# Kernel tuning notes

Hardware: AMD Instinct MI355X
Metric: run time of the kernel (lower is better)

## Reference

```python
import jax, jax.numpy as jnp
import numpy as np

T, H, F, E, K = 4096, 2048, 1408, 8, 2  # tokens, hidden, intermediate, experts, top_k


def setup_inputs() -> dict:
    key = jax.random.key(0)
    k1, k2, k3, k4 = jax.random.split(key, 4)
    return {
        "hidden_states": jax.random.normal(k1, (T, H), dtype=jnp.float32),
        "router_logits": jax.random.normal(k2, (T, E), dtype=jnp.float32),
        # w1: (E, 2, H, F) where dim 1 = [gate_proj, up_proj]
        "w1": jax.random.normal(k3, (E, 2, H, F), dtype=jnp.float32) * 0.02,
        # w2: (E, F, H) down projection
        "w2": jax.random.normal(k4, (E, F, H), dtype=jnp.float32) * 0.02,
        "top_k": K,
    }


def reference(hidden_states, router_logits, w1, w2, top_k):
    # Router: softmax over all experts, then select top_k.
    # renormalize_topk_logits=False -> combine weights are the raw softmax probs.
    probs = jax.nn.softmax(router_logits, axis=-1)            # (T, E)
    topk_w, topk_ids = jax.lax.top_k(probs, top_k)            # (T, K) each

    num_experts = w1.shape[0]
    out = jnp.zeros_like(hidden_states)                       # (T, H)
    # Fixed small loop over experts (structurally distinct weight slices);
    # each expert's FFN is a dense GEMM over all tokens, masked by the
    # per-token combine coefficient (0 for tokens not routed to this expert).
    for e in range(num_experts):
        coef = jnp.sum(jnp.where(topk_ids == e, topk_w, 0.0), axis=-1)  # (T,)
        gate = hidden_states @ w1[e, 0]                       # (T, F)
        up = hidden_states @ w1[e, 1]                         # (T, F)
        h = jax.nn.silu(gate) * up                            # SwiGLU
        out = out + coef[:, None] * (h @ w2[e])               # (T, H)
    return out
```

## Files before the change

### kernel.cpp

```cpp
#include <hip/hip_runtime.h>
#include <stdint.h>

#define T_TOK 4096
#define HID   2048
#define FF    1408
#define NE    8
#define BUF   16384
#define NT1   (HID / 32)
#define NT2   (FF / 32)

typedef __attribute__((ext_vector_type(8))) short short8;
typedef __attribute__((ext_vector_type(4))) float f32x4;

__device__ inline unsigned short f2bf(float f) {
  uint32_t u = __builtin_bit_cast(uint32_t, f);
  u += 0x7fffu + ((u >> 16) & 1u);
  return (unsigned short)(u >> 16);
}

__device__ inline uint32_t cvt_pk(float a, float b) {
  uint32_t r;
  asm("v_cvt_pk_bf16_f32 %0, %1, %2" : "=v"(r) : "v"(a), "v"(b));
  return r;
}

__device__ inline void gload16(const void* g, void* l) {
  __builtin_amdgcn_global_load_lds(
      (const __attribute__((address_space(1))) unsigned int*)g,
      (__attribute__((address_space(3))) unsigned int*)l, 16, 0, 0);
}

__device__ inline void wait8_barrier() {
  asm volatile("s_waitcnt vmcnt(8)" ::: "memory");
  __builtin_amdgcn_s_barrier();
  asm volatile("" ::: "memory");
}
__device__ inline void wait4_barrier() {
  asm volatile("s_waitcnt vmcnt(4)" ::: "memory");
  __builtin_amdgcn_s_barrier();
  asm volatile("" ::: "memory");
}
__device__ inline void wait0_barrier() {
  asm volatile("s_waitcnt vmcnt(0)" ::: "memory");
  __builtin_amdgcn_s_barrier();
  asm volatile("" ::: "memory");
}

__global__ __launch_bounds__(256) void route_kernel(const float* __restrict__ logits,
                                                    int2* __restrict__ eids,
                                                    float2* __restrict__ ecfs) {
  int t = blockIdx.x * 256 + threadIdx.x;
  const float4* lp = (const float4*)(logits + (size_t)t * NE);
  float4 a = lp[0], b = lp[1];
  float l[8] = {a.x, a.y, a.z, a.w, b.x, b.y, b.z, b.w};
  float mx = l[0];
#pragma unroll
  for (int i = 1; i < 8; ++i) mx = fmaxf(mx, l[i]);
  float s = 0.f, p[8];
#pragma unroll
  for (int i = 0; i < 8; ++i) { p[i] = __expf(l[i] - mx); s += p[i]; }
  float inv = 1.f / s;
  int e0 = 0;
#pragma unroll
  for (int i = 1; i < 8; ++i) if (l[i] > l[e0]) e0 = i;
  int e1 = (e0 == 0) ? 1 : 0;
#pragma unroll
  for (int i = 0; i < 8; ++i) if (i != e0 && l[i] > l[e1]) e1 = i;
  eids[t] = make_int2(e0, e1);
  ecfs[t] = make_float2(p[e0] * inv, p[e1] * inv);
}

__global__ __launch_bounds__(256) void compact_kernel(const int2* __restrict__ eids,
                                                      const float2* __restrict__ ecfs,
                                                      int* __restrict__ tok,
                                                      float* __restrict__ coef,
                                                      int* __restrict__ rowptr,
                                                      int* __restrict__ invm) {
  int e = blockIdx.x, tid = threadIdx.x;
  __shared__ int hist[8];
  __shared__ int wsum[4];
  __shared__ int runv;
  if (tid < 8) hist[tid] = 0;
  __syncthreads();
  for (int t = tid; t < T_TOK; t += 256) {
    int2 ei = eids[t];
    atomicAdd(&hist[ei.x], 1);
    atomicAdd(&hist[ei.y], 1);
  }
  __syncthreads();
  int off = 0;
  for (int j = 0; j < e; ++j) off += hist[j];
  if (tid == 0) {
    runv = 0;
    if (e == 0) rowptr[0] = 0;
    rowptr[e + 1] = off + hist[e];
  }
  __syncthreads();
  int wave = tid >> 6, lane = tid & 63;
  for (int c = 0; c < T_TOK; c += 256) {
    int t = c + tid;
    int2 ei = eids[t];
    float2 cf = ecfs[t];
    bool fl = false; float cv = 0.f; int ks = 0;
    if (ei.x == e)      { fl = true; cv = cf.x; ks = 0; }
    else if (ei.y == e) { fl = true; cv = cf.y; ks = 1; }
    unsigned long long m = __ballot(fl);
    if (lane == 0) wsum[wave] = __popcll(m);
    __syncthreads();
    int woff = runv;
    for (int wv = 0; wv < wave; ++wv) woff += wsum[wv];
    int pos = off + woff + __popcll(m & ((1ull << lane) - 1ull));
    if (fl) { tok[pos] = t; coef[pos] = cv; invm[2 * t + ks] = pos; }
    __syncthreads();
    if (tid == 0) runv += wsum[0] + wsum[1] + wsum[2] + wsum[3];
    __syncthreads();
  }
}

__global__ __launch_bounds__(256) void cvtx_kernel(const float* __restrict__ x,
                                                   unsigned short* __restrict__ xb) {
  int i = blockIdx.x * 256 + threadIdx.x;
  float4 v = ((const float4*)x)[i];
  uint2 o;
  o.x = cvt_pk(v.x, v.y);
  o.y = cvt_pk(v.z, v.w);
  ((uint2*)xb)[i] = o;
}

__global__ __launch_bounds__(256) void wcvt_kernel(const float* __restrict__ in,
                                                   unsigned short* __restrict__ out,
                                                   int R, int C) {
  __shared__ unsigned short t[64][72];
  const float* ip = in + ((size_t)blockIdx.z * R + blockIdx.y * 64) * C + blockIdx.x * 64;
  int tid = threadIdx.x;
  int r = tid >> 2, cg = (tid & 3) * 16;
  const float* rp = ip + (size_t)r * C + cg;
#pragma unroll
  for (int j = 0; j < 4; ++j) {
    float4 v = *(const float4*)(rp + j * 4);
    int c = cg + j * 4;
    t[c + 0][r] = f2bf(v.x);
    t[c + 1][r] = f2bf(v.y);
    t[c + 2][r] = f2bf(v.z);
    t[c + 3][r] = f2bf(v.w);
  }
  __syncthreads();
  int cr = tid >> 2, kg = (tid & 3) * 16;
  unsigned short* op = out + ((size_t)blockIdx.z * C + blockIdx.x * 64 + cr) * R +
                       blockIdx.y * 64 + kg;
  *(short8*)op = *(const short8*)&t[cr][kg];
  *(short8*)(op + 8) = *(const short8*)&t[cr][kg + 8];
}

__global__ __launch_bounds__(256) void gemm1_kernel(const unsigned short* __restrict__ Xb,
                                                    const unsigned short* __restrict__ w1t,
                                                    const int* __restrict__ tok,
                                                    const int* __restrict__ rowptr,
                                                    unsigned short* __restrict__ hbuf) {
  int f = blockIdx.x + 22 * blockIdx.y;
  int g = (f & 7) * 88 + (f >> 3);
  int ftile = g >> 5, mtile = g & 31;
  int e = blockIdx.z;
  int base = rowptr[e], cnt = rowptr[e + 1] - base;
  if (mtile * 128 >= cnt) return;
  __shared__ char smem[4 * BUF];
  int tid = threadIdx.x, lane = tid & 63, wave = tid >> 6;

  int rA = wave * 32 + (lane >> 2);
  int cd = (lane & 3) ^ ((rA >> 1) & 3);
  int sA0 = min(mtile * 128 + rA, cnt - 1);
  int sA1 = min(mtile * 128 + rA + 16, cnt - 1);
  const unsigned short* gA0 = Xb + (size_t)tok[base + sA0] * HID + cd * 8;
  const unsigned short* gA1 = Xb + (size_t)tok[base + sA1] * HID + cd * 8;
  int r1 = rA + 16;
  int p0 = (rA >> 4) & 1, f0 = (rA & 15) + 16 * (rA >> 5);
  int p1 = (r1 >> 4) & 1, f1 = (r1 & 15) + 16 * (r1 >> 5);
  const unsigned short* gB0 = w1t + ((size_t)(e * 2 + p0) * FF + ftile * 64 + f0) * HID + cd * 8;
  const unsigned short* gB1 = w1t + ((size_t)(e * 2 + p1) * FF + ftile * 64 + f1) * HID + cd * 8;
  int lb = wave * 2048 + lane * 16;

#define STG1(bp, k0) do {                          \
    gload16(gA0 + (k0), (bp) + lb);                \
    gload16(gA1 + (k0), (bp) + lb + 1024);         \
    gload16(gB0 + (k0), (bp) + 8192 + lb);         \
    gload16(gB1 + (k0), (bp) + 8192 + lb + 1024);  \
  } while (0)

  int wm = wave >> 1, wn = wave & 1, kc = lane >> 4;
  int aoff[4], boff[4];
#pragma unroll
  for (int mi = 0; mi < 4; ++mi) {
    int row = wm * 64 + mi * 16 + (lane & 15);
    aoff[mi] = row * 64 + ((kc ^ ((row >> 1) & 3)) << 4);
  }
#pragma unroll
  for (int ni = 0; ni < 4; ++ni) {
    int n = wn * 64 + ni * 16 + (lane & 15);
    boff[ni] = 8192 + n * 64 + ((kc ^ ((n >> 1) & 3)) << 4);
  }

  const f32x4 vz = {0.f, 0.f, 0.f, 0.f};
  f32x4 acc[4][4];
#pragma unroll
  for (int mi = 0; mi < 4; ++mi)
#pragma unroll
    for (int ni = 0; ni < 4; ++ni) acc[mi][ni] = vz;

  STG1(smem, 0);
  STG1(smem + BUF, 32);
  STG1(smem + 2 * BUF, 64);
  wait8_barrier();

  for (int t = 0; t < NT1; ++t) {
    char* cur = smem + (t & 3) * BUF;
    bool pf = (t + 3) < NT1;
    if (pf) STG1(smem + ((t + 3) & 3) * BUF, (t + 3) * 32);
    short8 af[4], bb[4];
#pragma unroll
    for (int mi = 0; mi < 4; ++mi) af[mi] = *(const short8*)(cur + aoff[mi]);
#pragma unroll
    for (int ni = 0; ni < 4; ++ni) bb[ni] = *(const short8*)(cur + boff[ni]);
    __builtin_amdgcn_s_setprio(1);
#pragma unroll
    for (int mi = 0; mi < 4; ++mi)
#pragma unroll
      for (int ni = 0; ni < 4; ++ni)
        acc[mi][ni] = __builtin_amdgcn_mfma_f32_16x16x32_bf16(af[mi], bb[ni], acc[mi][ni], 0, 0, 0);
    __builtin_amdgcn_s_setprio(0);
    if (pf) wait8_barrier();
    else if (t + 2 < NT1) wait4_barrier();
    else wait0_barrier();
  }
#undef STG1

  int fb = ftile * 64 + wn * 32 + (lane & 15);
#pragma unroll
  for (int mi = 0; mi < 4; ++mi) {
#pragma unroll
    for (int i = 0; i < 4; ++i) {
      int ml = wm * 64 + mi * 16 + (lane >> 4) * 4 + i;
      int slot = mtile * 128 + ml;
      if (slot < cnt) {
        size_t hrow = (size_t)(base + slot) * FF + fb;
        float g0 = acc[mi][0][i], u0 = acc[mi][1][i];
        float g1 = acc[mi][2][i], u1 = acc[mi][3][i];
        hbuf[hrow]      = f2bf(g0 / (1.f + __expf(-g0)) * u0);
        hbuf[hrow + 16] = f2bf(g1 / (1.f + __expf(-g1)) * u1);
      }
    }
  }
}

__global__ __launch_bounds__(256) void gemm2_kernel(const unsigned short* __restrict__ hbuf,
                                                    const unsigned short* __restrict__ w2t,
                                                    const int* __restrict__ rowptr,
                                                    float* __restrict__ obuf) {
  int f = blockIdx.x + 16 * blockIdx.y;
  int g = (f & 7) * 64 + (f >> 3);
  int ntile = g >> 5, mtile = g & 31;
  int e = blockIdx.z;
  int base = rowptr[e], cnt = rowptr[e + 1] - base;
  if (mtile * 128 >= cnt) return;
  __shared__ char smem[3 * BUF];
  int tid = threadIdx.x, lane = tid & 63, wave = tid >> 6;

  int rA = wave * 32 + (lane >> 2);
  int cd = (lane & 3) ^ ((rA >> 1) & 3);
  int sA0 = min(mtile * 128 + rA, cnt - 1);
  int sA1 = min(mtile * 128 + rA + 16, cnt - 1);
  const unsigned short* gA0 = hbuf + (size_t)(base + sA0) * FF + cd * 8;
  const unsigned short* gA1 = hbuf + (size_t)(base + sA1) * FF + cd * 8;
  const unsigned short* gB0 = w2t + ((size_t)e * HID + ntile * 128 + rA) * FF + cd * 8;
  const unsigned short* gB1 = gB0 + (size_t)16 * FF;
  int lb = wave * 2048 + lane * 16;

#define STG2(bp, k0) do {                          \
    gload16(gA0 + (k0), (bp) + lb);                \
    gload16(gA1 + (k0), (bp) + lb + 1024);         \
    gload16(gB0 + (k0), (bp) + 8192 + lb);         \
    gload16(gB1 + (k0), (bp) + 8192 + lb + 1024);  \
  } while (0)

  int wm = wave >> 1, wn = wave & 1, kc = lane >> 4;
  int aoff[4], boff[4];
#pragma unroll
  for (int mi = 0; mi < 4; ++mi) {
    int row = wm * 64 + mi * 16 + (lane & 15);
    aoff[mi] = row * 64 + ((kc ^ ((row >> 1) & 3)) << 4);
  }
#pragma unroll
  for (int ni = 0; ni < 4; ++ni) {
    int n = wn * 64 + ni * 16 + (lane & 15);
    boff[ni] = 8192 + n * 64 + ((kc ^ ((n >> 1) & 3)) << 4);
  }

  const f32x4 vz = {0.f, 0.f, 0.f, 0.f};
  f32x4 acc[4][4];
#pragma unroll
  for (int mi = 0; mi < 4; ++mi)
#pragma unroll
    for (int ni = 0; ni < 4; ++ni) acc[mi][ni] = vz;

  STG2(smem, 0);
  STG2(smem + BUF, 32);
  wait4_barrier();

  char* cur = smem;
  char* nxt = smem + 2 * BUF;
  for (int t = 0; t < NT2; ++t) {
    bool pf = (t + 2) < NT2;
    if (pf) STG2(nxt, (t + 2) * 32);
    short8 af[4], bb[4];
#pragma unroll
    for (int mi = 0; mi < 4; ++mi) af[mi] = *(const short8*)(cur + aoff[mi]);
#pragma unroll
    for (int ni = 0; ni < 4; ++ni) bb[ni] = *(const short8*)(cur + boff[ni]);
    __builtin_amdgcn_s_setprio(1);
#pragma unroll
    for (int mi = 0; mi < 4; ++mi)
#pragma unroll
      for (int ni = 0; ni < 4; ++ni)
        acc[mi][ni] = __builtin_amdgcn_mfma_f32_16x16x32_bf16(af[mi], bb[ni], acc[mi][ni], 0, 0, 0);
    __builtin_amdgcn_s_setprio(0);
    if (pf) wait4_barrier(); else wait0_barrier();
    cur = (cur == smem + 2 * BUF) ? smem : cur + BUF;
    nxt = (nxt == smem + 2 * BUF) ? smem : nxt + BUF;
  }
#undef STG2

  int nb = ntile * 128 + wn * 64 + (lane & 15);
#pragma unroll
  for (int mi = 0; mi < 4; ++mi) {
#pragma unroll
    for (int i = 0; i < 4; ++i) {
      int ml = wm * 64 + mi * 16 + (lane >> 4) * 4 + i;
      int slot = mtile * 128 + ml;
      if (slot < cnt) {
        float* op = obuf + (size_t)(base + slot) * HID + nb;
#pragma unroll
        for (int ni = 0; ni < 4; ++ni) op[ni * 16] = acc[mi][ni][i];
      }
    }
  }
}

__global__ __launch_bounds__(256) void combine_kernel(const float* __restrict__ obuf,
                                                      const int2* __restrict__ invm,
                                                      const float* __restrict__ coef,
                                                      float* __restrict__ out) {
  int idx = blockIdx.x * 256 + threadIdx.x;
  int t = idx >> 9, h4 = idx & 511;
  int2 pp = invm[t];
  float c0 = coef[pp.x], c1 = coef[pp.y];
  float4 a = ((const float4*)(obuf + (size_t)pp.x * HID))[h4];
  float4 b = ((const float4*)(obuf + (size_t)pp.y * HID))[h4];
  float4 o;
  o.x = c0 * a.x + c1 * b.x;
  o.y = c0 * a.y + c1 * b.y;
  o.z = c0 * a.z + c1 * b.z;
  o.w = c0 * a.w + c1 * b.w;
  ((float4*)out)[idx] = o;
}

__global__ __launch_bounds__(256) void gemm2_atomic(const unsigned short* __restrict__ hbuf,
                                                    const unsigned short* __restrict__ w2t,
                                                    const int* __restrict__ tok,
                                                    const float* __restrict__ coef,
                                                    const int* __restrict__ rowptr,
                                                    float* __restrict__ out) {
  int f = blockIdx.x + 16 * blockIdx.y;
  int g = (f & 7) * 64 + (f >> 3);
  int ntile = g >> 5, mtile = g & 31;
  int e = blockIdx.z;
  int base = rowptr[e], cnt = rowptr[e + 1] - base;
  if (mtile * 128 >= cnt) return;
  __shared__ char smem[3 * BUF];
  __shared__ int tokL[128];
  __shared__ float cofL[128];
  int tid = threadIdx.x, lane = tid & 63, wave = tid >> 6;
  if (tid < 128) {
    int slot = min(mtile * 128 + tid, cnt - 1);
    tokL[tid] = tok[base + slot];
    cofL[tid] = coef[base + slot];
  }
  __syncthreads();

  int rA = wave * 32 + (lane >> 2);
  int cd = (lane & 3) ^ ((rA >> 1) & 3);
  int sA0 = min(mtile * 128 + rA, cnt - 1);
  int sA1 = min(mtile * 128 + rA + 16, cnt - 1);
  const unsigned short* gA0 = hbuf + (size_t)(base + sA0) * FF + cd * 8;
  const unsigned short* gA1 = hbuf + (size_t)(base + sA1) * FF + cd * 8;
  const unsigned short* gB0 = w2t + ((size_t)e * HID + ntile * 128 + rA) * FF + cd * 8;
  const unsigned short* gB1 = gB0 + (size_t)16 * FF;
  int lb = wave * 2048 + lane * 16;

#define STG2F(bp, k0) do {                         \
    gload16(gA0 + (k0), (bp) + lb);                \
    gload16(gA1 + (k0), (bp) + lb + 1024);         \
    gload16(gB0 + (k0), (bp) + 8192 + lb);         \
    gload16(gB1 + (k0), (bp) + 8192 + lb + 1024);  \
  } while (0)

  int wm = wave >> 1, wn = wave & 1, kc = lane >> 4;
  int aoff[4], boff[4];
#pragma unroll
  for (int mi = 0; mi < 4; ++mi) {
    int row = wm * 64 + mi * 16 + (lane & 15);
    aoff[mi] = row * 64 + ((kc ^ ((row >> 1) & 3)) << 4);
  }
#pragma unroll
  for (int ni = 0; ni < 4; ++ni) {
    int n = wn * 64 + ni * 16 + (lane & 15);
    boff[ni] = 8192 + n * 64 + ((kc ^ ((n >> 1) & 3)) << 4);
  }

  const f32x4 vz = {0.f, 0.f, 0.f, 0.f};
  f32x4 acc[4][4];
#pragma unroll
  for (int mi = 0; mi < 4; ++mi)
#pragma unroll
    for (int ni = 0; ni < 4; ++ni) acc[mi][ni] = vz;

  STG2F(smem, 0);
  STG2F(smem + BUF, 32);
  wait4_barrier();

  char* cur = smem;
  char* nxt = smem + 2 * BUF;
  for (int t = 0; t < NT2; ++t) {
    bool pf = (t + 2) < NT2;
    if (pf) STG2F(nxt, (t + 2) * 32);
    short8 af[4], bb[4];
#pragma unroll
    for (int mi = 0; mi < 4; ++mi) af[mi] = *(const short8*)(cur + aoff[mi]);
#pragma unroll
    for (int ni = 0; ni < 4; ++ni) bb[ni] = *(const short8*)(cur + boff[ni]);
    __builtin_amdgcn_s_setprio(1);
#pragma unroll
    for (int mi = 0; mi < 4; ++mi)
#pragma unroll
      for (int ni = 0; ni < 4; ++ni)
        acc[mi][ni] = __builtin_amdgcn_mfma_f32_16x16x32_bf16(af[mi], bb[ni], acc[mi][ni], 0, 0, 0);
    __builtin_amdgcn_s_setprio(0);
    if (pf) wait4_barrier(); else wait0_barrier();
    cur = (cur == smem + 2 * BUF) ? smem : cur + BUF;
    nxt = (nxt == smem + 2 * BUF) ? smem : nxt + BUF;
  }
#undef STG2F

#pragma unroll
  for (int mi = 0; mi < 4; ++mi) {
#pragma unroll
    for (int i = 0; i < 4; ++i) {
      int ml = wm * 64 + mi * 16 + (lane >> 4) * 4 + i;
      int slot = mtile * 128 + ml;
      if (slot < cnt) {
        float cf = cofL[ml];
        float* op = out + (size_t)tokL[ml] * HID + ntile * 128 + wn * 64 + (lane & 15);
#pragma unroll
        for (int ni = 0; ni < 4; ++ni)
          unsafeAtomicAdd(op + ni * 16, cf * acc[mi][ni][i]);
      }
    }
  }
}

extern "C" void kernel_launch(void* const* d_in, const int* in_sizes, int n_in,
                              void* d_out, int out_size, void* d_ws, size_t ws_size,
                              hipStream_t stream) {
  const float* X  = (const float*)d_in[0];
  const float* RL = (const float*)d_in[1];
  const float* W1 = (const float*)d_in[2];
  const float* W2 = (const float*)d_in[3];
  float* out = (float*)d_out;

  const size_t OFF_EIDS = 4096;
  const size_t OFF_ECFS = 36864;
  const size_t OFF_TOK  = 69632;
  const size_t OFF_COEF = 102400;
  const size_t OFF_XB   = 135168;
  const size_t OFF_H    = 16912384;
  const size_t OFF_W1T  = 39981056;
  const size_t OFF_W2T  = 132255744;
  const size_t TOTAL2   = 178393088;
  const size_t OFF_INV  = 178393088;
  const size_t TOTAL3   = 178425856;
  if (ws_size < TOTAL2 || n_in < 4) return;
  bool big = ws_size >= TOTAL3;

  char* w = (char*)d_ws;
  int*    rowptr = (int*)w;
  int2*   eids   = (int2*)(w + OFF_EIDS);
  float2* ecfs   = (float2*)(w + OFF_ECFS);
  int*    tok    = (int*)(w + OFF_TOK);
  float*  coef   = (float*)(w + OFF_COEF);
  unsigned short* Xb   = (unsigned short*)(w + OFF_XB);
  unsigned short* hbuf = (unsigned short*)(w + OFF_H);
  unsigned short* w1t  = (unsigned short*)(w + OFF_W1T);
  unsigned short* w2t  = (unsigned short*)(w + OFF_W2T);
  float* obuf = (float*)(w + OFF_W1T);
  int* invm = big ? (int*)(w + OFF_INV) : (int*)hbuf;

  if (!big) hipMemsetAsync(d_out, 0, (size_t)T_TOK * HID * sizeof(float), stream);
  route_kernel<<<T_TOK / 256, 256, 0, stream>>>(RL, eids, ecfs);
  compact_kernel<<<NE, 256, 0, stream>>>(eids, ecfs, tok, coef, rowptr, invm);
  cvtx_kernel<<<(T_TOK * HID / 4) / 256, 256, 0, stream>>>(X, Xb);
  wcvt_kernel<<<dim3(FF / 64, HID / 64, NE * 2), 256, 0, stream>>>(W1, w1t, HID, FF);
  wcvt_kernel<<<dim3(HID / 64, FF / 64, NE), 256, 0, stream>>>(W2, w2t, FF, HID);
  gemm1_kernel<<<dim3(FF / 64, T_TOK / 128, NE), 256, 0, stream>>>(Xb, w1t, tok, rowptr, hbuf);
  if (big) {
    gemm2_kernel<<<dim3(HID / 128, T_TOK / 128, NE), 256, 0, stream>>>(hbuf, w2t, rowptr, obuf);
    combine_kernel<<<(T_TOK * HID / 4) / 256, 256, 0, stream>>>(obuf, (const int2*)invm, coef, out);
  } else {
    gemm2_atomic<<<dim3(HID / 128, T_TOK / 128, NE), 256, 0, stream>>>(hbuf, w2t, tok, coef, rowptr, out);
  }
}
```

Measured before the change: 345.6 us.

## Enlarge gemm1 tile to 256 rows with 512 threads and K=64 steps

Restructures the grouped first GEMM to use 512-thread blocks computing 256x64 (gate/up interleaved) tiles with K-steps of 64 over a 3-stage LDS ring, splitting each step into two half-MFMA phases with loads interleaved between barriers. The goal is more reuse of weight tiles per token row, fewer loop iterations and barriers, and overlap of global-to-LDS loads with MFMA. It uses about 144KB LDS with one block per CU, which lowers occupancy, adds barriers inside each step, and wastes more work on partially filled 256-row tiles.

New measurement: 363.5 us. +5.2%, slower.

```diff
diff --git a/kernel.cpp b/kernel.cpp
--- a/kernel.cpp
+++ b/kernel.cpp
@@ -6,8 +6,9 @@
 #define FF    1408
 #define NE    8
 #define BUF   16384
-#define NT1   (HID / 32)
 #define NT2   (FF / 32)
+#define NKT1  (HID / 64)
+#define SL1   49152
 
 typedef __attribute__((ext_vector_type(8))) short short8;
 typedef __attribute__((ext_vector_type(4))) float f32x4;
@@ -30,11 +31,6 @@
       (__attribute__((address_space(3))) unsigned int*)l, 16, 0, 0);
 }
 
-__device__ inline void wait8_barrier() {
-  asm volatile("s_waitcnt vmcnt(8)" ::: "memory");
-  __builtin_amdgcn_s_barrier();
-  asm volatile("" ::: "memory");
-}
 __device__ inline void wait4_barrier() {
   asm volatile("s_waitcnt vmcnt(4)" ::: "memory");
   __builtin_amdgcn_s_barrier();
@@ -152,51 +148,52 @@
   *(short8*)(op + 8) = *(const short8*)&t[cr][kg + 8];
 }
 
-__global__ __launch_bounds__(256) void gemm1_kernel(const unsigned short* __restrict__ Xb,
-                                                    const unsigned short* __restrict__ w1t,
-                                                    const int* __restrict__ tok,
-                                                    const int* __restrict__ rowptr,
-                                                    unsigned short* __restrict__ hbuf) {
-  int f = blockIdx.x + 22 * blockIdx.y;
-  int g = (f & 7) * 88 + (f >> 3);
-  int ftile = g >> 5, mtile = g & 31;
+__global__ __launch_bounds__(512, 1) void gemm1_kernel(const unsigned short* __restrict__ Xb,
+                                                       const unsigned short* __restrict__ w1t,
+                                                       const int* __restrict__ tok,
+                                                       const int* __restrict__ rowptr,
+                                                       unsigned short* __restrict__ hbuf) {
   int e = blockIdx.z;
+  int f = blockIdx.x + 8 * blockIdx.y;
+  int g = (f & 7) * 22 + (f >> 3);
+  int ftile = g >> 3, mtile = g & 7;
   int base = rowptr[e], cnt = rowptr[e + 1] - base;
-  if (mtile * 128 >= cnt) return;
-  __shared__ char smem[4 * BUF];
+  if (mtile * 256 >= cnt) return;
+  __shared__ char smem[3 * SL1];
   int tid = threadIdx.x, lane = tid & 63, wave = tid >> 6;
-
-  int rA = wave * 32 + (lane >> 2);
-  int cd = (lane & 3) ^ ((rA >> 1) & 3);
-  int sA0 = min(mtile * 128 + rA, cnt - 1);
-  int sA1 = min(mtile * 128 + rA + 16, cnt - 1);
-  const unsigned short* gA0 = Xb + (size_t)tok[base + sA0] * HID + cd * 8;
-  const unsigned short* gA1 = Xb + (size_t)tok[base + sA1] * HID + cd * 8;
-  int r1 = rA + 16;
-  int p0 = (rA >> 4) & 1, f0 = (rA & 15) + 16 * (rA >> 5);
-  int p1 = (r1 >> 4) & 1, f1 = (r1 & 15) + 16 * (r1 >> 5);
-  const unsigned short* gB0 = w1t + ((size_t)(e * 2 + p0) * FF + ftile * 64 + f0) * HID + cd * 8;
-  const unsigned short* gB1 = w1t + ((size_t)(e * 2 + p1) * FF + ftile * 64 + f1) * HID + cd * 8;
-  int lb = wave * 2048 + lane * 16;
-
-#define STG1(bp, k0) do {                          \
-    gload16(gA0 + (k0), (bp) + lb);                \
-    gload16(gA1 + (k0), (bp) + lb + 1024);         \
-    gload16(gB0 + (k0), (bp) + 8192 + lb);         \
-    gload16(gB1 + (k0), (bp) + 8192 + lb + 1024);  \
-  } while (0)
-
-  int wm = wave >> 1, wn = wave & 1, kc = lane >> 4;
+  int wm = wave >> 1, wn = wave & 1;
+
+  int p = tid & 7, rr = tid >> 3;
+  const unsigned short* gA[4];
+  const unsigned short* gB[2];
+#pragma unroll
+  for (int c = 0; c < 4; ++c) {
+    int row = 64 * c + rr;
+    int ch = p ^ (row & 7);
+    int slot = min(mtile * 256 + row, cnt - 1);
+    gA[c] = Xb + (size_t)tok[base + slot] * HID + ch * 8;
+  }
+#pragma unroll
+  for (int c = 0; c < 2; ++c) {
+    int row = 64 * c + rr;
+    int ch = p ^ (row & 7);
+    int proj = (row >> 4) & 1;
+    int fg = ftile * 64 + (row & 15) + 16 * (row >> 5);
+    gB[c] = w1t + ((size_t)(e * 2 + proj) * FF + fg) * HID + ch * 8;
+  }
+  int ldst = tid * 16;
+
+  int gq = lane >> 4, j = lane & 15;
   int aoff[4], boff[4];
 #pragma unroll
   for (int mi = 0; mi < 4; ++mi) {
-    int row = wm * 64 + mi * 16 + (lane & 15);
-    aoff[mi] = row * 64 + ((kc ^ ((row >> 1) & 3)) << 4);
+    int row = wm * 64 + mi * 16 + j;
+    aoff[mi] = row * 128 + ((gq ^ (row & 7)) << 4);
   }
 #pragma unroll
   for (int ni = 0; ni < 4; ++ni) {
-    int n = wn * 64 + ni * 16 + (lane & 15);
-    boff[ni] = 8192 + n * 64 + ((kc ^ ((n >> 1) & 3)) << 4);
+    int row = wn * 64 + ni * 16 + j;
+    boff[ni] = 32768 + row * 128 + ((gq ^ (row & 7)) << 4);
   }
 
   const f32x4 vz = {0.f, 0.f, 0.f, 0.f};
@@ -206,46 +203,95 @@
 #pragma unroll
     for (int ni = 0; ni < 4; ++ni) acc[mi][ni] = vz;
 
-  STG1(smem, 0);
-  STG1(smem + BUF, 32);
-  STG1(smem + 2 * BUF, 64);
-  wait8_barrier();
-
-  for (int t = 0; t < NT1; ++t) {
-    char* cur = smem + (t & 3) * BUF;
-    bool pf = (t + 3) < NT1;
-    if (pf) STG1(smem + ((t + 3) & 3) * BUF, (t + 3) * 32);
-    short8 af[4], bb[4];
-#pragma unroll
-    for (int mi = 0; mi < 4; ++mi) af[mi] = *(const short8*)(cur + aoff[mi]);
-#pragma unroll
-    for (int ni = 0; ni < 4; ++ni) bb[ni] = *(const short8*)(cur + boff[ni]);
+  gload16(gA[0], smem + ldst);
+  gload16(gA[1], smem + 8192 + ldst);
+  gload16(gA[2], smem + 16384 + ldst);
+  gload16(gA[3], smem + 24576 + ldst);
+  gload16(gB[0], smem + 32768 + ldst);
+  gload16(gB[1], smem + 40960 + ldst);
+  gload16(gA[0] + 64, smem + SL1 + ldst);
+  gload16(gA[1] + 64, smem + SL1 + 8192 + ldst);
+  gload16(gA[2] + 64, smem + SL1 + 16384 + ldst);
+  gload16(gA[3] + 64, smem + SL1 + 24576 + ldst);
+  gload16(gB[0] + 64, smem + SL1 + 32768 + ldst);
+  gload16(gB[1] + 64, smem + SL1 + 40960 + ldst);
+  asm volatile("s_waitcnt vmcnt(6)" ::: "memory");
+  __builtin_amdgcn_s_barrier();
+
+  for (int t = 0; t < NKT1; ++t) {
+    const char* S = smem + (t % 3) * SL1;
+    char* P = smem + ((t + 2) % 3) * SL1;
+    bool pf = (t + 2) < NKT1;
+    int kn = (t + 2) * 64;
+    short8 bb[4][2];
+#pragma unroll
+    for (int ni = 0; ni < 4; ++ni) {
+      bb[ni][0] = *(const short8*)(S + boff[ni]);
+      bb[ni][1] = *(const short8*)(S + (boff[ni] ^ 64));
+    }
+    short8 af[2][2];
+#pragma unroll
+    for (int mi = 0; mi < 2; ++mi) {
+      af[mi][0] = *(const short8*)(S + aoff[mi]);
+      af[mi][1] = *(const short8*)(S + (aoff[mi] ^ 64));
+    }
+    if (pf) {
+      gload16(gA[0] + kn, P + ldst);
+      gload16(gA[1] + kn, P + 8192 + ldst);
+      gload16(gA[2] + kn, P + 16384 + ldst);
+    }
+    __builtin_amdgcn_s_barrier();
     __builtin_amdgcn_s_setprio(1);
 #pragma unroll
-    for (int mi = 0; mi < 4; ++mi)
-#pragma unroll
-      for (int ni = 0; ni < 4; ++ni)
-        acc[mi][ni] = __builtin_amdgcn_mfma_f32_16x16x32_bf16(af[mi], bb[ni], acc[mi][ni], 0, 0, 0);
+    for (int mi = 0; mi < 2; ++mi)
+#pragma unroll
+      for (int ni = 0; ni < 4; ++ni) {
+        acc[mi][ni] = __builtin_amdgcn_mfma_f32_16x16x32_bf16(af[mi][0], bb[ni][0], acc[mi][ni], 0, 0, 0);
+        acc[mi][ni] = __builtin_amdgcn_mfma_f32_16x16x32_bf16(af[mi][1], bb[ni][1], acc[mi][ni], 0, 0, 0);
+      }
     __builtin_amdgcn_s_setprio(0);
-    if (pf) wait8_barrier();
-    else if (t + 2 < NT1) wait4_barrier();
-    else wait0_barrier();
-  }
-#undef STG1
-
-  int fb = ftile * 64 + wn * 32 + (lane & 15);
+    __builtin_amdgcn_s_barrier();
+    short8 ag[2][2];
+#pragma unroll
+    for (int mi = 0; mi < 2; ++mi) {
+      ag[mi][0] = *(const short8*)(S + aoff[2 + mi]);
+      ag[mi][1] = *(const short8*)(S + (aoff[2 + mi] ^ 64));
+    }
+    if (pf) {
+      gload16(gA[3] + kn, P + 24576 + ldst);
+      gload16(gB[0] + kn, P + 32768 + ldst);
+      gload16(gB[1] + kn, P + 40960 + ldst);
+    }
+    __builtin_amdgcn_s_barrier();
+    __builtin_amdgcn_s_setprio(1);
+#pragma unroll
+    for (int mi = 0; mi < 2; ++mi)
+#pragma unroll
+      for (int ni = 0; ni < 4; ++ni) {
+        acc[2 + mi][ni] = __builtin_amdgcn_mfma_f32_16x16x32_bf16(ag[mi][0], bb[ni][0], acc[2 + mi][ni], 0, 0, 0);
+        acc[2 + mi][ni] = __builtin_amdgcn_mfma_f32_16x16x32_bf16(ag[mi][1], bb[ni][1], acc[2 + mi][ni], 0, 0, 0);
+      }
+    __builtin_amdgcn_s_setprio(0);
+    if (pf) asm volatile("s_waitcnt vmcnt(6)" ::: "memory");
+    else    asm volatile("s_waitcnt vmcnt(0)" ::: "memory");
+    __builtin_amdgcn_s_barrier();
+  }
+
+  int fb = ftile * 64 + j;
 #pragma unroll
   for (int mi = 0; mi < 4; ++mi) {
 #pragma unroll
     for (int i = 0; i < 4; ++i) {
-      int ml = wm * 64 + mi * 16 + (lane >> 4) * 4 + i;
-      int slot = mtile * 128 + ml;
+      int ml = wm * 64 + mi * 16 + gq * 4 + i;
+      int slot = mtile * 256 + ml;
       if (slot < cnt) {
         size_t hrow = (size_t)(base + slot) * FF + fb;
-        float g0 = acc[mi][0][i], u0 = acc[mi][1][i];
-        float g1 = acc[mi][2][i], u1 = acc[mi][3][i];
-        hbuf[hrow]      = f2bf(g0 / (1.f + __expf(-g0)) * u0);
-        hbuf[hrow + 16] = f2bf(g1 / (1.f + __expf(-g1)) * u1);
+#pragma unroll
+        for (int pr = 0; pr < 2; ++pr) {
+          float gg = acc[mi][2 * pr][i], uu = acc[mi][2 * pr + 1][i];
+          float hv = gg / (1.f + __expf(-gg)) * uu;
+          hbuf[hrow + 16 * (2 * wn + pr)] = f2bf(hv);
+        }
       }
     }
   }
@@ -508,7 +554,7 @@
   cvtx_kernel<<<(T_TOK * HID / 4) / 256, 256, 0, stream>>>(X, Xb);
   wcvt_kernel<<<dim3(FF / 64, HID / 64, NE * 2), 256, 0, stream>>>(W1, w1t, HID, FF);
   wcvt_kernel<<<dim3(HID / 64, FF / 64, NE), 256, 0, stream>>>(W2, w2t, FF, HID);
-  gemm1_kernel<<<dim3(FF / 64, T_TOK / 128, NE), 256, 0, stream>>>(Xb, w1t, tok, rowptr, hbuf);
+  gemm1_kernel<<<dim3(8, 22, NE), 512, 0, stream>>>(Xb, w1t, tok, rowptr, hbuf);
   if (big) {
     gemm2_kernel<<<dim3(HID / 128, T_TOK / 128, NE), 256, 0, stream>>>(hbuf, w2t, rowptr, obuf);
     combine_kernel<<<(T_TOK * HID / 4) / 256, 256, 0, stream>>>(obuf, (const int2*)invm, coef, out);
```

## Fuse routing into compaction and interleave W2 conversion with gemm1 blocks

Applied to the files above, without the earlier changes.

Removes the separate routing kernel by recomputing softmax/top-2 inline inside the compaction kernel, which now reads the logits twice per expert block. It also merges the W2 transpose/bf16 conversion into the gemm1 launch: half the blocks of a 1D grid do W2 conversion tiles while the other half run gemm1 tiles, so the memory-bound conversion overlaps the compute-bound GEMM. This saves launches and lets both kinds of work share the device, at the cost of redundant routing math and a more complex block index mapping.

After: 437.5 us. 26.6% more time.

```diff
diff --git a/kernel.cpp b/kernel.cpp
--- a/kernel.cpp
+++ b/kernel.cpp
@@ -46,12 +46,9 @@
   asm volatile("" ::: "memory");
 }
 
-__global__ __launch_bounds__(256) void route_kernel(const float* __restrict__ logits,
-                                                    int2* __restrict__ eids,
-                                                    float2* __restrict__ ecfs) {
-  int t = blockIdx.x * 256 + threadIdx.x;
-  const float4* lp = (const float4*)(logits + (size_t)t * NE);
-  float4 a = lp[0], b = lp[1];
+__device__ inline void route1(const float* __restrict__ lp, int& e0, int& e1,
+                              float& c0, float& c1) {
+  float4 a = ((const float4*)lp)[0], b = ((const float4*)lp)[1];
   float l[8] = {a.x, a.y, a.z, a.w, b.x, b.y, b.z, b.w};
   float mx = l[0];
 #pragma unroll
@@ -60,18 +57,17 @@
 #pragma unroll
   for (int i = 0; i < 8; ++i) { p[i] = __expf(l[i] - mx); s += p[i]; }
   float inv = 1.f / s;
-  int e0 = 0;
+  e0 = 0;
 #pragma unroll
   for (int i = 1; i < 8; ++i) if (l[i] > l[e0]) e0 = i;
-  int e1 = (e0 == 0) ? 1 : 0;
+  e1 = (e0 == 0) ? 1 : 0;
 #pragma unroll
   for (int i = 0; i < 8; ++i) if (i != e0 && l[i] > l[e1]) e1 = i;
-  eids[t] = make_int2(e0, e1);
-  ecfs[t] = make_float2(p[e0] * inv, p[e1] * inv);
-}
-
-__global__ __launch_bounds__(256) void compact_kernel(const int2* __restrict__ eids,
-                                                      const float2* __restrict__ ecfs,
+  c0 = p[e0] * inv;
+  c1 = p[e1] * inv;
+}
+
+__global__ __launch_bounds__(256) void compact_kernel(const float* __restrict__ logits,
                                                       int* __restrict__ tok,
                                                       float* __restrict__ coef,
                                                       int* __restrict__ rowptr,
@@ -83,9 +79,10 @@
   if (tid < 8) hist[tid] = 0;
   __syncthreads();
   for (int t = tid; t < T_TOK; t += 256) {
-    int2 ei = eids[t];
-    atomicAdd(&hist[ei.x], 1);
-    atomicAdd(&hist[ei.y], 1);
+    int e0, e1; float c0, c1;
+    route1(logits + (size_t)t * NE, e0, e1, c0, c1);
+    atomicAdd(&hist[e0], 1);
+    atomicAdd(&hist[e1], 1);
   }
   __syncthreads();
   int off = 0;
@@ -99,11 +96,11 @@
   int wave = tid >> 6, lane = tid & 63;
   for (int c = 0; c < T_TOK; c += 256) {
     int t = c + tid;
-    int2 ei = eids[t];
-    float2 cf = ecfs[t];
+    int e0, e1; float c0, c1;
+    route1(logits + (size_t)t * NE, e0, e1, c0, c1);
     bool fl = false; float cv = 0.f; int ks = 0;
-    if (ei.x == e)      { fl = true; cv = cf.x; ks = 0; }
-    else if (ei.y == e) { fl = true; cv = cf.y; ks = 1; }
+    if (e0 == e)      { fl = true; cv = c0; ks = 0; }
+    else if (e1 == e) { fl = true; cv = c1; ks = 1; }
     unsigned long long m = __ballot(fl);
     if (lane == 0) wsum[wave] = __popcll(m);
     __syncthreads();
@@ -152,19 +149,52 @@
   *(short8*)(op + 8) = *(const short8*)&t[cr][kg + 8];
 }
 
-__global__ __launch_bounds__(256) void gemm1_kernel(const unsigned short* __restrict__ Xb,
-                                                    const unsigned short* __restrict__ w1t,
-                                                    const int* __restrict__ tok,
-                                                    const int* __restrict__ rowptr,
-                                                    unsigned short* __restrict__ hbuf) {
-  int f = blockIdx.x + 22 * blockIdx.y;
+__global__ __launch_bounds__(256) void gemm1_fused(const unsigned short* __restrict__ Xb,
+                                                   const unsigned short* __restrict__ w1t,
+                                                   const int* __restrict__ tok,
+                                                   const int* __restrict__ rowptr,
+                                                   unsigned short* __restrict__ hbuf,
+                                                   const float* __restrict__ W2,
+                                                   unsigned short* __restrict__ w2t) {
+  __shared__ char smem[4 * BUF];
+  int bid = blockIdx.x;
+  int tid = threadIdx.x;
+  int sub = bid & 15;
+
+  if (sub >= 8) {
+    int wv = (bid >> 4) * 8 + (sub - 8);
+    int bx = wv & 31;
+    int by = (wv >> 5) % 22;
+    int bz = wv / 704;
+    unsigned short (*t)[72] = (unsigned short (*)[72])smem;
+    const float* ip = W2 + ((size_t)bz * FF + by * 64) * HID + bx * 64;
+    int r = tid >> 2, cg = (tid & 3) * 16;
+    const float* rp = ip + (size_t)r * HID + cg;
+#pragma unroll
+    for (int j = 0; j < 4; ++j) {
+      float4 v = *(const float4*)(rp + j * 4);
+      int c = cg + j * 4;
+      t[c + 0][r] = f2bf(v.x);
+      t[c + 1][r] = f2bf(v.y);
+      t[c + 2][r] = f2bf(v.z);
+      t[c + 3][r] = f2bf(v.w);
+    }
+    __syncthreads();
+    int cr = tid >> 2, kg = (tid & 3) * 16;
+    unsigned short* op = w2t + ((size_t)bz * HID + bx * 64 + cr) * FF + by * 64 + kg;
+    *(short8*)op = *(const short8*)&t[cr][kg];
+    *(short8*)(op + 8) = *(const short8*)&t[cr][kg + 8];
+    return;
+  }
+
+  int g1 = (bid >> 4) * 8 + sub;
+  int e = g1 / 704;
+  int f = g1 % 704;
   int g = (f & 7) * 88 + (f >> 3);
   int ftile = g >> 5, mtile = g & 31;
-  int e = blockIdx.z;
   int base = rowptr[e], cnt = rowptr[e + 1] - base;
   if (mtile * 128 >= cnt) return;
-  __shared__ char smem[4 * BUF];
-  int tid = threadIdx.x, lane = tid & 63, wave = tid >> 6;
+  int lane = tid & 63, wave = tid >> 6;
 
   int rA = wave * 32 + (lane >> 2);
   int cd = (lane & 3) ^ ((rA >> 1) & 3);
@@ -475,8 +505,6 @@
   const float* W2 = (const float*)d_in[3];
   float* out = (float*)d_out;
 
-  const size_t OFF_EIDS = 4096;
-  const size_t OFF_ECFS = 36864;
   const size_t OFF_TOK  = 69632;
   const size_t OFF_COEF = 102400;
   const size_t OFF_XB   = 135168;
@@ -491,8 +519,6 @@
 
   char* w = (char*)d_ws;
   int*    rowptr = (int*)w;
-  int2*   eids   = (int2*)(w + OFF_EIDS);
-  float2* ecfs   = (float2*)(w + OFF_ECFS);
   int*    tok    = (int*)(w + OFF_TOK);
   float*  coef   = (float*)(w + OFF_COEF);
   unsigned short* Xb   = (unsigned short*)(w + OFF_XB);
@@ -503,12 +529,10 @@
   int* invm = big ? (int*)(w + OFF_INV) : (int*)hbuf;
 
   if (!big) hipMemsetAsync(d_out, 0, (size_t)T_TOK * HID * sizeof(float), stream);
-  route_kernel<<<T_TOK / 256, 256, 0, stream>>>(RL, eids, ecfs);
-  compact_kernel<<<NE, 256, 0, stream>>>(eids, ecfs, tok, coef, rowptr, invm);
+  compact_kernel<<<NE, 256, 0, stream>>>(RL, tok, coef, rowptr, invm);
   cvtx_kernel<<<(T_TOK * HID / 4) / 256, 256, 0, stream>>>(X, Xb);
   wcvt_kernel<<<dim3(FF / 64, HID / 64, NE * 2), 256, 0, stream>>>(W1, w1t, HID, FF);
-  wcvt_kernel<<<dim3(HID / 64, FF / 64, NE), 256, 0, stream>>>(W2, w2t, FF, HID);
-  gemm1_kernel<<<dim3(FF / 64, T_TOK / 128, NE), 256, 0, stream>>>(Xb, w1t, tok, rowptr, hbuf);
+  gemm1_fused<<<11264, 256, 0, stream>>>(Xb, w1t, tok, rowptr, hbuf, W2, w2t);
   if (big) {
     gemm2_kernel<<<dim3(HID / 128, T_TOK / 128, NE), 256, 0, stream>>>(hbuf, w2t, rowptr, obuf);
     combine_kernel<<<(T_TOK * HID / 4) / 256, 256, 0, stream>>>(obuf, (const int2*)invm, coef, out);
```
